# Kernel tuning notes

Measured on AMD Instinct MI355X. Metric: run time of the kernel, lower is better.

The kernel has to match this reference:

```python
import jax, jax.numpy as jnp
import numpy as np

COV_EMB = 32
N_HEAD = 2
FACTOR_TCL = 2   # TemporalConvolutionalLayer factor (default 2)
FACTOR_MLP = 1   # MLP factor passed from MultiAttention init
EPS = 1e-5


def _conv1d_causal(x, w, b):
    # x: [N, C, T], w: [O, C, 3]; torch pads 2 both sides then slices [..., :-2],
    # equivalent to left-pad 2 only -> output length T.
    y = jax.lax.conv_general_dilated(x, w, window_strides=(1,), padding=[(2, 0)],
                                     dimension_numbers=('NCH', 'OIH', 'NCH'))
    return y + b[None, :, None]


def _tcl(x, w_conv, b_conv, w_proj, b_proj):
    # TemporalConvolutionalLayer: x [..., T, C] -> [..., T, C]
    shp = x.shape
    T, C = shp[-2], shp[-1]
    x2 = x.reshape(-1, T, C).transpose(0, 2, 1)              # [N, C, T]
    h = jax.nn.gelu(_conv1d_causal(x2, w_conv, b_conv), approximate=False)
    h = h.transpose(0, 2, 1)                                  # [N, T, 2C]
    out = h @ w_proj.T + b_proj                               # [N, T, C]
    return out.reshape(*shp[:-1], C)


def _layernorm(x, w):
    mu = jnp.mean(x, axis=-1, keepdims=True)
    var = jnp.var(x, axis=-1, keepdims=True)
    return (x - mu) * jax.lax.rsqrt(var + EPS) * w


def setup_inputs() -> dict:
    key = jax.random.key(0)
    ks = jax.random.split(key, 20)
    C = COV_EMB
    C2 = FACTOR_TCL * C
    s = 0.02
    inp = {
        'causal_decoder': jax.random.normal(ks[0], (8, 4, 1024, C), jnp.float32),
        'past_kv': jax.random.normal(ks[1], (8, 1024, C), jnp.float32),
    }
    def tcl_params(i):
        return (jax.random.normal(ks[i], (C2, C, 3), jnp.float32) * s,
                jnp.zeros((C2,), jnp.float32),
                jax.random.normal(ks[i + 1], (C, C2), jnp.float32) * s,
                jnp.zeros((C,), jnp.float32))
    inp['wq_conv'], inp['bq_conv'], inp['wq_proj'], inp['bq_proj'] = tcl_params(2)
    inp['wk_conv'], inp['bk_conv'], inp['wk_proj'], inp['bk_proj'] = tcl_params(4)
    inp['wv_conv'], inp['bv_conv'], inp['wv_proj'], inp['bv_proj'] = tcl_params(6)
    inp['w_cproj'] = jax.random.normal(ks[8], (C, C), jnp.float32) * s   # bias=False
    inp['ln_w'] = jnp.ones((C,), jnp.float32)                            # bias=False
    inp['w_fc'] = jax.random.normal(ks[9], (FACTOR_MLP * C, C), jnp.float32) * s   # bias=False
    inp['w_mlp_proj'] = jax.random.normal(ks[10], (C, FACTOR_MLP * C), jnp.float32) * s
    return inp


def reference(causal_decoder, past_kv,
              wq_conv, bq_conv, wq_proj, bq_proj,
              wk_conv, bk_conv, wk_proj, bk_proj,
              wv_conv, bv_conv, wv_proj, bv_proj,
              w_cproj, ln_w, w_fc, w_mlp_proj):
    B, F, T, C = causal_decoder.shape
    nh, hd = N_HEAD, C // N_HEAD

    q = _tcl(causal_decoder, wq_conv, bq_conv, wq_proj, bq_proj)   # [B,F,T,C]
    k = _tcl(past_kv, wk_conv, bk_conv, wk_proj, bk_proj)          # [B,S,C]
    v = _tcl(past_kv, wv_conv, bv_conv, wv_proj, bv_proj)          # [B,S,C]

    S = k.shape[1]
    q = q.reshape(B, F, T, nh, hd).transpose(0, 1, 3, 2, 4)        # [B,F,h,T,d]
    k = k.reshape(B, S, nh, hd).transpose(0, 2, 1, 3)              # [B,h,S,d]
    v = v.reshape(B, S, nh, hd).transpose(0, 2, 1, 3)              # [B,h,S,d]

    scale = 1.0 / jnp.sqrt(jnp.asarray(hd, q.dtype))
    scores = jnp.einsum('bfhtd,bhsd->bfhts', q, k) * scale          # [B,F,h,T,S]
    attn = jax.nn.softmax(scores, axis=-1)
    y = jnp.einsum('bfhts,bhsd->bfhtd', attn, v)                    # [B,F,h,T,d]
    y = y.transpose(0, 1, 3, 2, 4).reshape(B, F, T, C)

    out = causal_decoder + y @ w_cproj.T                            # resid_dropout = id (p=0)
    h = _layernorm(out, ln_w)
    mlp = jax.nn.gelu(h @ w_fc.T, approximate=False) @ w_mlp_proj.T
    out = out + mlp
    return out
```

## Files before the change

### kernel.cpp

```cpp
#include <hip/hip_runtime.h>

#define T_LEN 1024

typedef __attribute__((ext_vector_type(8))) short short8;
typedef __attribute__((ext_vector_type(4))) short short4v;
typedef __attribute__((ext_vector_type(4))) float float4v;

__device__ __forceinline__ float gelu_exact(float x) {
    return 0.5f * x * (1.0f + erff(x * 0.70710678118654752440f));
}
__device__ __forceinline__ unsigned short f2bf(float f) {
    unsigned u = __float_as_uint(f);
    u += 0x7fffu + ((u >> 16) & 1u);
    return (unsigned short)(u >> 16);
}

__global__ __launch_bounds__(256) void tcl_mfma(
    const float* __restrict__ cd, const float* __restrict__ pkv,
    const float* __restrict__ wqc, const float* __restrict__ bqc,
    const float* __restrict__ wqp, const float* __restrict__ bqp,
    const float* __restrict__ wkc, const float* __restrict__ bkc,
    const float* __restrict__ wkp, const float* __restrict__ bkp,
    const float* __restrict__ wvc, const float* __restrict__ bvc,
    const float* __restrict__ wvp, const float* __restrict__ bvp,
    unsigned short* __restrict__ qbf, unsigned short* __restrict__ kbf,
    unsigned short* __restrict__ vtbf)
{
    __shared__ __align__(16) unsigned short Abuf[64 * 96];
    __shared__ __align__(16) unsigned short WbT[64 * 96];
    __shared__ __align__(16) unsigned short Hb[64 * 72];
    __shared__ __align__(16) unsigned short WpB[32 * 72];

    const int tid = threadIdx.x;
    const int gb = blockIdx.x;

    const float *src, *wc, *bc, *wp, *bp;
    unsigned short* outb;
    int n, mode;
    if (gb < 512)      { n = gb >> 4;          src = cd;  wc = wqc; bc = bqc; wp = wqp; bp = bqp; outb = qbf;  mode = 0; }
    else if (gb < 640) { n = (gb - 512) >> 4;  src = pkv; wc = wkc; bc = bkc; wp = wkp; bp = bkp; outb = kbf;  mode = 0; }
    else               { n = (gb - 640) >> 4;  src = pkv; wc = wvc; bc = bvc; wp = wvp; bp = bvp; outb = vtbf; mode = 1; }
    const int t0 = (gb & 15) * 64;

#pragma unroll
    for (int it = 0; it < 6; ++it) {
        int s = (tid + it * 256) >> 3;
        int sub = tid & 7;
        int t = s / 3, tap = s - t * 3;
        int tau = t0 + t - 2 + tap;
        float4 xv = make_float4(0.f, 0.f, 0.f, 0.f);
        if (tau >= 0) xv = *(const float4*)&src[((size_t)n * T_LEN + tau) * 32 + sub * 4];
        short4v pk = { (short)f2bf(xv.x), (short)f2bf(xv.y),
                       (short)f2bf(xv.z), (short)f2bf(xv.w) };
        *(short4v*)&Abuf[t * 96 + tap * 32 + sub * 4] = pk;
    }
#pragma unroll
    for (int it = 0; it < 6; ++it) {
        int i4 = tid + it * 256;
        int idx = i4 * 4;
        int o = idx / 96, r = idx - o * 96;
        float4 w4 = *(const float4*)&wc[idx];
        float we[4] = { w4.x, w4.y, w4.z, w4.w };
#pragma unroll
        for (int e = 0; e < 4; ++e) {
            int re = r + e, c = re / 3, tap = re - c * 3;
            WbT[o * 96 + tap * 32 + c] = f2bf(we[e]);
        }
    }
#pragma unroll
    for (int it = 0; it < 2; ++it) {
        int i4 = tid + it * 256;
        int idx = i4 * 4;
        int c = idx >> 6, o = idx & 63;
        float4 w4 = *(const float4*)&wp[idx];
        short4v pk = { (short)f2bf(w4.x), (short)f2bf(w4.y),
                       (short)f2bf(w4.z), (short)f2bf(w4.w) };
        *(short4v*)&WpB[c * 72 + o] = pk;
    }

    const int w = tid >> 6;
    const int ln = tid & 63;
    const int sn = ln & 15;
    const int quad = ln >> 4;

    const float bcv = bc[w * 16 + sn];
    const float bp0 = bp[sn], bp1 = bp[16 + sn];

    __syncthreads();

    short8 b0 = *(const short8*)&WbT[(w * 16 + sn) * 96 + 0  + quad * 8];
    short8 b1 = *(const short8*)&WbT[(w * 16 + sn) * 96 + 32 + quad * 8];
    short8 b2 = *(const short8*)&WbT[(w * 16 + sn) * 96 + 64 + quad * 8];
    float4v zero = { 0.f, 0.f, 0.f, 0.f };
    float4v acc[4] = { zero, zero, zero, zero };
#pragma unroll
    for (int tm = 0; tm < 4; ++tm) {
        const unsigned short* ar = &Abuf[(tm * 16 + sn) * 96 + quad * 8];
        short8 a0 = *(const short8*)(ar + 0);
        short8 a1 = *(const short8*)(ar + 32);
        short8 a2 = *(const short8*)(ar + 64);
        acc[tm] = __builtin_amdgcn_mfma_f32_16x16x32_bf16(a0, b0, acc[tm], 0, 0, 0);
        acc[tm] = __builtin_amdgcn_mfma_f32_16x16x32_bf16(a1, b1, acc[tm], 0, 0, 0);
        acc[tm] = __builtin_amdgcn_mfma_f32_16x16x32_bf16(a2, b2, acc[tm], 0, 0, 0);
    }
#pragma unroll
    for (int tm = 0; tm < 4; ++tm) {
        float ge[4];
        ge[0] = gelu_exact(acc[tm].x + bcv);
        ge[1] = gelu_exact(acc[tm].y + bcv);
        ge[2] = gelu_exact(acc[tm].z + bcv);
        ge[3] = gelu_exact(acc[tm].w + bcv);
#pragma unroll
        for (int i = 0; i < 4; ++i)
            Hb[(tm * 16 + quad * 4 + i) * 72 + w * 16 + sn] = f2bf(ge[i]);
    }

    __syncthreads();

    const unsigned short* hr = &Hb[(w * 16 + sn) * 72 + quad * 8];
    short8 pa0 = *(const short8*)(hr + 0);
    short8 pa1 = *(const short8*)(hr + 32);
    short8 pb00 = *(const short8*)&WpB[sn * 72 + quad * 8];
    short8 pb01 = *(const short8*)&WpB[sn * 72 + 32 + quad * 8];
    short8 pb10 = *(const short8*)&WpB[(16 + sn) * 72 + quad * 8];
    short8 pb11 = *(const short8*)&WpB[(16 + sn) * 72 + 32 + quad * 8];
    float4v acc0 = zero, acc1 = zero;
    acc0 = __builtin_amdgcn_mfma_f32_16x16x32_bf16(pa0, pb00, acc0, 0, 0, 0);
    acc0 = __builtin_amdgcn_mfma_f32_16x16x32_bf16(pa1, pb01, acc0, 0, 0, 0);
    acc1 = __builtin_amdgcn_mfma_f32_16x16x32_bf16(pa0, pb10, acc1, 0, 0, 0);
    acc1 = __builtin_amdgcn_mfma_f32_16x16x32_bf16(pa1, pb11, acc1, 0, 0, 0);

    float v0[4] = { acc0.x + bp0, acc0.y + bp0, acc0.z + bp0, acc0.w + bp0 };
    float v1[4] = { acc1.x + bp1, acc1.y + bp1, acc1.z + bp1, acc1.w + bp1 };
#pragma unroll
    for (int i = 0; i < 4; ++i) {
        int t = w * 16 + quad * 4 + i;
        if (mode == 0) {
            size_t rowb = ((size_t)n * T_LEN + t0 + t) * 32;
            outb[rowb + sn]      = f2bf(v0[i]);
            outb[rowb + 16 + sn] = f2bf(v1[i]);
        } else {
            outb[((size_t)(n * 2 + 0) * 16 + sn) * T_LEN + t0 + t] = f2bf(v0[i]);
            outb[((size_t)(n * 2 + 1) * 16 + sn) * T_LEN + t0 + t] = f2bf(v1[i]);
        }
    }
}

__global__ __launch_bounds__(256) void attn_kernel(
    const unsigned short* __restrict__ qbf,
    const unsigned short* __restrict__ kbf,
    const unsigned short* __restrict__ vtbf,
    float* __restrict__ yws)
{
    __shared__ unsigned short plds[4 * 16 * 36];

    const int tid = threadIdx.x;
    const int w = tid >> 6;
    const int ln = tid & 63;
    const int sn = ln & 15;
    const int quad = ln >> 4;
    const int g = blockIdx.x;
    const int tt = g & 15;
    const int bfh = g >> 4;
    const int h = bfh & 1;
    const int bf = bfh >> 1;
    const int b = bf >> 2;
    const int trow = tt * 64 + w * 16 + sn;

    short8 aq = {0, 0, 0, 0, 0, 0, 0, 0};
    if (quad < 2)
        aq = *(const short8*)(qbf + ((size_t)bf * T_LEN + trow) * 32 + h * 16 + quad * 8);

    const unsigned short* kb = kbf + (size_t)b * T_LEN * 32 + h * 16 + quad * 8;
    const unsigned short* vb = vtbf + ((size_t)(b * 2 + h) * 16 + sn) * T_LEN + quad * 8;
    unsigned short* pw = plds + w * 576;

    float4v yacc = {0.f, 0.f, 0.f, 0.f};
    float l0 = 0.f, l1 = 0.f, l2 = 0.f, l3 = 0.f;
    const float SC = 0.36067376022224085f;

#pragma unroll 1
    for (int s0 = 0; s0 < 1024; s0 += 32) {
        short8 bk0 = {0, 0, 0, 0, 0, 0, 0, 0};
        short8 bk1 = {0, 0, 0, 0, 0, 0, 0, 0};
        if (quad < 2) {
            bk0 = *(const short8*)(kb + (size_t)(s0 + sn) * 32);
            bk1 = *(const short8*)(kb + (size_t)(s0 + 16 + sn) * 32);
        }
        float4v z = {0.f, 0.f, 0.f, 0.f};
        float4v c0 = __builtin_amdgcn_mfma_f32_16x16x32_bf16(aq, bk0, z, 0, 0, 0);
        float4v c1 = __builtin_amdgcn_mfma_f32_16x16x32_bf16(aq, bk1, z, 0, 0, 0);

        float p00 = exp2f(c0.x * SC), p01 = exp2f(c0.y * SC);
        float p02 = exp2f(c0.z * SC), p03 = exp2f(c0.w * SC);
        float p10 = exp2f(c1.x * SC), p11 = exp2f(c1.y * SC);
        float p12 = exp2f(c1.z * SC), p13 = exp2f(c1.w * SC);
        l0 += p00 + p10; l1 += p01 + p11;
        l2 += p02 + p12; l3 += p03 + p13;

        const int tb = quad * 4;
        pw[(tb + 0) * 36 + sn]      = f2bf(p00);
        pw[(tb + 1) * 36 + sn]      = f2bf(p01);
        pw[(tb + 2) * 36 + sn]      = f2bf(p02);
        pw[(tb + 3) * 36 + sn]      = f2bf(p03);
        pw[(tb + 0) * 36 + 16 + sn] = f2bf(p10);
        pw[(tb + 1) * 36 + 16 + sn] = f2bf(p11);
        pw[(tb + 2) * 36 + 16 + sn] = f2bf(p12);
        pw[(tb + 3) * 36 + 16 + sn] = f2bf(p13);

        const unsigned short* pr = pw + sn * 36 + quad * 8;
        short4v plo = *(const short4v*)pr;
        short4v phi = *(const short4v*)(pr + 4);
        short8 ap = {plo.x, plo.y, plo.z, plo.w, phi.x, phi.y, phi.z, phi.w};

        short8 bv = *(const short8*)(vb + s0);
        yacc = __builtin_amdgcn_mfma_f32_16x16x32_bf16(ap, bv, yacc, 0, 0, 0);
    }

#pragma unroll
    for (int off = 1; off < 16; off <<= 1) {
        l0 += __shfl_xor(l0, off); l1 += __shfl_xor(l1, off);
        l2 += __shfl_xor(l2, off); l3 += __shfl_xor(l3, off);
    }
    const float i0 = 1.f / l0, i1 = 1.f / l1, i2 = 1.f / l2, i3 = 1.f / l3;

    float* yp = yws + ((size_t)bf * T_LEN + tt * 64 + w * 16 + quad * 4) * 32 + h * 16 + sn;
    yp[0 * 32] = yacc.x * i0;
    yp[1 * 32] = yacc.y * i1;
    yp[2 * 32] = yacc.z * i2;
    yp[3 * 32] = yacc.w * i3;
}

__global__ __launch_bounds__(256) void epi_kernel(
    const float* __restrict__ cd, const float* __restrict__ yws,
    const float* __restrict__ wcp, const float* __restrict__ lnw,
    const float* __restrict__ wfc, const float* __restrict__ wmp,
    float* __restrict__ out)
{
    __shared__ float sy[64][32];
    __shared__ float shn[8][36], sg[8][36];
    __shared__ float sln[32];

    const int tid = threadIdx.x;
    const int rl = tid >> 5, c = tid & 31;

    float wa[32], wb[32], wm[32];
#pragma unroll
    for (int j4 = 0; j4 < 8; ++j4) {
        float4 a = *(const float4*)(wcp + c * 32 + j4 * 4);
        wa[j4 * 4 + 0] = a.x; wa[j4 * 4 + 1] = a.y; wa[j4 * 4 + 2] = a.z; wa[j4 * 4 + 3] = a.w;
        float4 f = *(const float4*)(wfc + c * 32 + j4 * 4);
        wb[j4 * 4 + 0] = f.x; wb[j4 * 4 + 1] = f.y; wb[j4 * 4 + 2] = f.z; wb[j4 * 4 + 3] = f.w;
        float4 m = *(const float4*)(wmp + c * 32 + j4 * 4);
        wm[j4 * 4 + 0] = m.x; wm[j4 * 4 + 1] = m.y; wm[j4 * 4 + 2] = m.z; wm[j4 * 4 + 3] = m.w;
    }
    if (tid < 32) sln[tid] = lnw[tid];

    const size_t base = (size_t)blockIdx.x * 64;
    {
        const float4* ysrc = (const float4*)(yws + base * 32);
        float4* ydst = (float4*)&sy[0][0];
        for (int i = tid; i < 512; i += 256) ydst[i] = ysrc[i];
    }
    __syncthreads();
    const float lnwc = sln[c];

#pragma unroll 1
    for (int p = 0; p < 8; ++p) {
        int r = p * 8 + rl;
        size_t row = base + r;
        float x1 = cd[row * 32 + c];
#pragma unroll
        for (int j4 = 0; j4 < 8; ++j4) {
            float4 yv = *(const float4*)&sy[r][j4 * 4];
            x1 += wa[j4 * 4 + 0] * yv.x + wa[j4 * 4 + 1] * yv.y +
                  wa[j4 * 4 + 2] * yv.z + wa[j4 * 4 + 3] * yv.w;
        }
        float s1 = x1, s2 = x1 * x1;
#pragma unroll
        for (int off = 16; off; off >>= 1) {
            s1 += __shfl_xor(s1, off);
            s2 += __shfl_xor(s2, off);
        }
        float mu = s1 * (1.0f / 32.0f);
        float var = s2 * (1.0f / 32.0f) - mu * mu;
        float hn = (x1 - mu) * rsqrtf(var + 1e-5f) * lnwc;
        shn[rl][c] = hn;
        float ga = 0.f;
#pragma unroll
        for (int j4 = 0; j4 < 8; ++j4) {
            float4 hv = *(const float4*)&shn[rl][j4 * 4];
            ga += wb[j4 * 4 + 0] * hv.x + wb[j4 * 4 + 1] * hv.y +
                  wb[j4 * 4 + 2] * hv.z + wb[j4 * 4 + 3] * hv.w;
        }
        float gv = gelu_exact(ga);
        sg[rl][c] = gv;
        float oa = x1;
#pragma unroll
        for (int j4 = 0; j4 < 8; ++j4) {
            float4 gvv = *(const float4*)&sg[rl][j4 * 4];
            oa += wm[j4 * 4 + 0] * gvv.x + wm[j4 * 4 + 1] * gvv.y +
                  wm[j4 * 4 + 2] * gvv.z + wm[j4 * 4 + 3] * gvv.w;
        }
        out[row * 32 + c] = oa;
    }
}

extern "C" void kernel_launch(void* const* d_in, const int* in_sizes, int n_in,
                              void* d_out, int out_size, void* d_ws, size_t ws_size,
                              hipStream_t stream) {
    const float* cd  = (const float*)d_in[0];
    const float* pkv = (const float*)d_in[1];
    const float* wqc = (const float*)d_in[2];
    const float* bqc = (const float*)d_in[3];
    const float* wqp = (const float*)d_in[4];
    const float* bqp = (const float*)d_in[5];
    const float* wkc = (const float*)d_in[6];
    const float* bkc = (const float*)d_in[7];
    const float* wkp = (const float*)d_in[8];
    const float* bkp = (const float*)d_in[9];
    const float* wvc = (const float*)d_in[10];
    const float* bvc = (const float*)d_in[11];
    const float* wvp = (const float*)d_in[12];
    const float* bvp = (const float*)d_in[13];
    const float* wcp = (const float*)d_in[14];
    const float* lnw = (const float*)d_in[15];
    const float* wfc = (const float*)d_in[16];
    const float* wmp = (const float*)d_in[17];

    unsigned short* qbf  = (unsigned short*)d_ws;
    unsigned short* kbf  = qbf + (size_t)32 * 1024 * 32;
    unsigned short* vtbf = kbf + (size_t)8 * 1024 * 32;
    float* yws = (float*)(vtbf + (size_t)8 * 1024 * 32);

    tcl_mfma<<<768, 256, 0, stream>>>(cd, pkv,
                                      wqc, bqc, wqp, bqp,
                                      wkc, bkc, wkp, bkp,
                                      wvc, bvc, wvp, bvp,
                                      qbf, kbf, vtbf);
    attn_kernel<<<1024, 256, 0, stream>>>(qbf, kbf, vtbf, yws);
    epi_kernel<<<512, 256, 0, stream>>>(cd, yws, wcp, lnw, wfc, wmp, (float*)d_out);
}
```

Before: 145.6 us.

## Split attention key range in two and merge partial sums in epilogue

The attention kernel now splits the 1024-long key dimension into two halves, so twice as many blocks (2048) each run half the loop. Each half writes unnormalized partial outputs and partial softmax denominators to workspace, and the epilogue kernel adds the two halves and normalizes. The aim is more parallelism and a shorter serial loop per block on the attention critical path. The cost is extra workspace traffic for the doubled y buffer plus the denominators. The merge by plain addition is exact only because no running-max subtraction is used.

```diff
diff --git a/kernel.cpp b/kernel.cpp
--- a/kernel.cpp
+++ b/kernel.cpp
@@ -150,7 +150,8 @@
     const unsigned short* __restrict__ qbf,
     const unsigned short* __restrict__ kbf,
     const unsigned short* __restrict__ vtbf,
-    float* __restrict__ yws)
+    float* __restrict__ ynws,
+    float* __restrict__ lws)
 {
     __shared__ unsigned short plds[4 * 16 * 36];
 
@@ -160,8 +161,9 @@
     const int sn = ln & 15;
     const int quad = ln >> 4;
     const int g = blockIdx.x;
-    const int tt = g & 15;
-    const int bfh = g >> 4;
+    const int half = g & 1;
+    const int tt = (g >> 1) & 15;
+    const int bfh = g >> 5;
     const int h = bfh & 1;
     const int bf = bfh >> 1;
     const int b = bf >> 2;
@@ -178,9 +180,10 @@
     float4v yacc = {0.f, 0.f, 0.f, 0.f};
     float l0 = 0.f, l1 = 0.f, l2 = 0.f, l3 = 0.f;
     const float SC = 0.36067376022224085f;
+    const int sbeg = half * 512;
 
 #pragma unroll 1
-    for (int s0 = 0; s0 < 1024; s0 += 32) {
+    for (int s0 = sbeg; s0 < sbeg + 512; s0 += 32) {
         short8 bk0 = {0, 0, 0, 0, 0, 0, 0, 0};
         short8 bk1 = {0, 0, 0, 0, 0, 0, 0, 0};
         if (quad < 2) {
@@ -222,17 +225,21 @@
         l0 += __shfl_xor(l0, off); l1 += __shfl_xor(l1, off);
         l2 += __shfl_xor(l2, off); l3 += __shfl_xor(l3, off);
     }
-    const float i0 = 1.f / l0, i1 = 1.f / l1, i2 = 1.f / l2, i3 = 1.f / l3;
-
-    float* yp = yws + ((size_t)bf * T_LEN + tt * 64 + w * 16 + quad * 4) * 32 + h * 16 + sn;
-    yp[0 * 32] = yacc.x * i0;
-    yp[1 * 32] = yacc.y * i1;
-    yp[2 * 32] = yacc.z * i2;
-    yp[3 * 32] = yacc.w * i3;
+
+    float* yp = ynws + (((size_t)half * 32 + bf) * T_LEN + tt * 64 + w * 16 + quad * 4) * 32 + h * 16 + sn;
+    yp[0 * 32] = yacc.x;
+    yp[1 * 32] = yacc.y;
+    yp[2 * 32] = yacc.z;
+    yp[3 * 32] = yacc.w;
+    if (sn == 0) {
+        float* lp = lws + (((size_t)half * 32 + bf) * 2 + h) * T_LEN + tt * 64 + w * 16 + quad * 4;
+        lp[0] = l0; lp[1] = l1; lp[2] = l2; lp[3] = l3;
+    }
 }
 
 __global__ __launch_bounds__(256) void epi_kernel(
-    const float* __restrict__ cd, const float* __restrict__ yws,
+    const float* __restrict__ cd, const float* __restrict__ ynws,
+    const float* __restrict__ lws,
     const float* __restrict__ wcp, const float* __restrict__ lnw,
     const float* __restrict__ wfc, const float* __restrict__ wmp,
     float* __restrict__ out)
@@ -256,11 +263,26 @@
     }
     if (tid < 32) sln[tid] = lnw[tid];
 
+    const int bf = blockIdx.x >> 4;
+    const int t0 = (blockIdx.x & 15) * 64;
     const size_t base = (size_t)blockIdx.x * 64;
     {
-        const float4* ysrc = (const float4*)(yws + base * 32);
+        const float4* yn0 = (const float4*)ynws;
+        const float4* yn1 = (const float4*)(ynws + (size_t)32 * T_LEN * 32);
         float4* ydst = (float4*)&sy[0][0];
-        for (int i = tid; i < 512; i += 256) ydst[i] = ysrc[i];
+        for (int i = tid; i < 512; i += 256) {
+            int r = i >> 3, c4 = i & 7, hh = c4 >> 2;
+            int t = t0 + r;
+            float l = lws[((size_t)bf * 2 + hh) * T_LEN + t] +
+                      lws[(((size_t)32 + bf) * 2 + hh) * T_LEN + t];
+            float inv = 1.0f / l;
+            float4 a = yn0[base * 8 + i];
+            float4 b = yn1[base * 8 + i];
+            float4 v;
+            v.x = (a.x + b.x) * inv; v.y = (a.y + b.y) * inv;
+            v.z = (a.z + b.z) * inv; v.w = (a.w + b.w) * inv;
+            ydst[i] = v;
+        }
     }
     __syncthreads();
     const float lnwc = sln[c];
@@ -331,13 +353,15 @@
     unsigned short* qbf  = (unsigned short*)d_ws;
     unsigned short* kbf  = qbf + (size_t)32 * 1024 * 32;
     unsigned short* vtbf = kbf + (size_t)8 * 1024 * 32;
-    float* yws = (float*)(vtbf + (size_t)8 * 1024 * 32);
+    float* ynws = (float*)(vtbf + (size_t)8 * 1024 * 32);
+    float* lws  = ynws + (size_t)2 * 32 * 1024 * 32;
 
     tcl_mfma<<<768, 256, 0, stream>>>(cd, pkv,
                                       wqc, bqc, wqp, bqp,
                                       wkc, bkc, wkp, bkp,
                                       wvc, bvc, wvp, bvp,
                                       qbf, kbf, vtbf);
-    attn_kernel<<<1024, 256, 0, stream>>>(qbf, kbf, vtbf, yws);
-    epi_kernel<<<512, 256, 0, stream>>>(cd, yws, wcp, lnw, wfc, wmp, (float*)d_out);
-}
+    attn_kernel<<<2048, 256, 0, stream>>>(qbf, kbf, vtbf, ynws, lws);
+    epi_kernel<<<512, 256, 0, stream>>>(cd, ynws, lws, wcp, lnw, wfc, wmp,
+                                        (float*)d_out);
+}
```

Measured after the change: 146.8 us. Within noise of the previous version (+0.9%).

## Halve TCL time tile to double blocks; unroll attention loop over 64 keys

Applied to the files above, without the earlier changes.

The TCL kernel now handles 32 time steps per block instead of 64, so it launches twice as many blocks. The projection GEMM work is split across the four waves by time-half and channel-half. The attention loop handles 64 keys per iteration, issuing four QK MFMAs and two PV MFMAs with separate LDS staging buffers so more loads and exps are in flight at once. The costs are that each TCL block reloads the conv weights for half the work, and the attention loop uses more registers and LDS.

```diff
diff --git a/kernel.cpp b/kernel.cpp
--- a/kernel.cpp
+++ b/kernel.cpp
@@ -26,9 +26,9 @@
     unsigned short* __restrict__ qbf, unsigned short* __restrict__ kbf,
     unsigned short* __restrict__ vtbf)
 {
-    __shared__ __align__(16) unsigned short Abuf[64 * 96];
+    __shared__ __align__(16) unsigned short Abuf[32 * 96];
     __shared__ __align__(16) unsigned short WbT[64 * 96];
-    __shared__ __align__(16) unsigned short Hb[64 * 72];
+    __shared__ __align__(16) unsigned short Hb[32 * 72];
     __shared__ __align__(16) unsigned short WpB[32 * 72];
 
     const int tid = threadIdx.x;
@@ -37,13 +37,13 @@
     const float *src, *wc, *bc, *wp, *bp;
     unsigned short* outb;
     int n, mode;
-    if (gb < 512)      { n = gb >> 4;          src = cd;  wc = wqc; bc = bqc; wp = wqp; bp = bqp; outb = qbf;  mode = 0; }
-    else if (gb < 640) { n = (gb - 512) >> 4;  src = pkv; wc = wkc; bc = bkc; wp = wkp; bp = bkp; outb = kbf;  mode = 0; }
-    else               { n = (gb - 640) >> 4;  src = pkv; wc = wvc; bc = bvc; wp = wvp; bp = bvp; outb = vtbf; mode = 1; }
-    const int t0 = (gb & 15) * 64;
-
-#pragma unroll
-    for (int it = 0; it < 6; ++it) {
+    if (gb < 1024)      { n = gb >> 5;           src = cd;  wc = wqc; bc = bqc; wp = wqp; bp = bqp; outb = qbf;  mode = 0; }
+    else if (gb < 1280) { n = (gb - 1024) >> 5;  src = pkv; wc = wkc; bc = bkc; wp = wkp; bp = bkp; outb = kbf;  mode = 0; }
+    else                { n = (gb - 1280) >> 5;  src = pkv; wc = wvc; bc = bvc; wp = wvp; bp = bvp; outb = vtbf; mode = 1; }
+    const int t0 = (gb & 31) * 32;
+
+#pragma unroll
+    for (int it = 0; it < 3; ++it) {
         int s = (tid + it * 256) >> 3;
         int sub = tid & 7;
         int t = s / 3, tap = s - t * 3;
@@ -84,7 +84,8 @@
     const int quad = ln >> 4;
 
     const float bcv = bc[w * 16 + sn];
-    const float bp0 = bp[sn], bp1 = bp[16 + sn];
+    const int tmw = w & 1, cnw = w >> 1;
+    const float bpv = bp[cnw * 16 + sn];
 
     __syncthreads();
 
@@ -92,9 +93,9 @@
     short8 b1 = *(const short8*)&WbT[(w * 16 + sn) * 96 + 32 + quad * 8];
     short8 b2 = *(const short8*)&WbT[(w * 16 + sn) * 96 + 64 + quad * 8];
     float4v zero = { 0.f, 0.f, 0.f, 0.f };
-    float4v acc[4] = { zero, zero, zero, zero };
-#pragma unroll
-    for (int tm = 0; tm < 4; ++tm) {
+    float4v acc[2] = { zero, zero };
+#pragma unroll
+    for (int tm = 0; tm < 2; ++tm) {
         const unsigned short* ar = &Abuf[(tm * 16 + sn) * 96 + quad * 8];
         short8 a0 = *(const short8*)(ar + 0);
         short8 a1 = *(const short8*)(ar + 32);
@@ -104,7 +105,7 @@
         acc[tm] = __builtin_amdgcn_mfma_f32_16x16x32_bf16(a2, b2, acc[tm], 0, 0, 0);
     }
 #pragma unroll
-    for (int tm = 0; tm < 4; ++tm) {
+    for (int tm = 0; tm < 2; ++tm) {
         float ge[4];
         ge[0] = gelu_exact(acc[tm].x + bcv);
         ge[1] = gelu_exact(acc[tm].y + bcv);
@@ -117,31 +118,24 @@
 
     __syncthreads();
 
-    const unsigned short* hr = &Hb[(w * 16 + sn) * 72 + quad * 8];
+    const unsigned short* hr = &Hb[(tmw * 16 + sn) * 72 + quad * 8];
     short8 pa0 = *(const short8*)(hr + 0);
     short8 pa1 = *(const short8*)(hr + 32);
-    short8 pb00 = *(const short8*)&WpB[sn * 72 + quad * 8];
-    short8 pb01 = *(const short8*)&WpB[sn * 72 + 32 + quad * 8];
-    short8 pb10 = *(const short8*)&WpB[(16 + sn) * 72 + quad * 8];
-    short8 pb11 = *(const short8*)&WpB[(16 + sn) * 72 + 32 + quad * 8];
-    float4v acc0 = zero, acc1 = zero;
-    acc0 = __builtin_amdgcn_mfma_f32_16x16x32_bf16(pa0, pb00, acc0, 0, 0, 0);
-    acc0 = __builtin_amdgcn_mfma_f32_16x16x32_bf16(pa1, pb01, acc0, 0, 0, 0);
-    acc1 = __builtin_amdgcn_mfma_f32_16x16x32_bf16(pa0, pb10, acc1, 0, 0, 0);
-    acc1 = __builtin_amdgcn_mfma_f32_16x16x32_bf16(pa1, pb11, acc1, 0, 0, 0);
-
-    float v0[4] = { acc0.x + bp0, acc0.y + bp0, acc0.z + bp0, acc0.w + bp0 };
-    float v1[4] = { acc1.x + bp1, acc1.y + bp1, acc1.z + bp1, acc1.w + bp1 };
+    short8 pb0 = *(const short8*)&WpB[(cnw * 16 + sn) * 72 + quad * 8];
+    short8 pb1 = *(const short8*)&WpB[(cnw * 16 + sn) * 72 + 32 + quad * 8];
+    float4v pacc = zero;
+    pacc = __builtin_amdgcn_mfma_f32_16x16x32_bf16(pa0, pb0, pacc, 0, 0, 0);
+    pacc = __builtin_amdgcn_mfma_f32_16x16x32_bf16(pa1, pb1, pacc, 0, 0, 0);
+
+    float v[4] = { pacc.x + bpv, pacc.y + bpv, pacc.z + bpv, pacc.w + bpv };
 #pragma unroll
     for (int i = 0; i < 4; ++i) {
-        int t = w * 16 + quad * 4 + i;
+        int t = tmw * 16 + quad * 4 + i;
+        int c = cnw * 16 + sn;
         if (mode == 0) {
-            size_t rowb = ((size_t)n * T_LEN + t0 + t) * 32;
-            outb[rowb + sn]      = f2bf(v0[i]);
-            outb[rowb + 16 + sn] = f2bf(v1[i]);
+            outb[((size_t)n * T_LEN + t0 + t) * 32 + c] = f2bf(v[i]);
         } else {
-            outb[((size_t)(n * 2 + 0) * 16 + sn) * T_LEN + t0 + t] = f2bf(v0[i]);
-            outb[((size_t)(n * 2 + 1) * 16 + sn) * T_LEN + t0 + t] = f2bf(v1[i]);
+            outb[((size_t)(n * 2 + cnw) * 16 + sn) * T_LEN + t0 + t] = f2bf(v[i]);
         }
     }
 }
@@ -152,7 +146,7 @@
     const unsigned short* __restrict__ vtbf,
     float* __restrict__ yws)
 {
-    __shared__ unsigned short plds[4 * 16 * 36];
+    __shared__ unsigned short plds[4 * 2 * 16 * 36];
 
     const int tid = threadIdx.x;
     const int w = tid >> 6;
@@ -173,48 +167,74 @@
 
     const unsigned short* kb = kbf + (size_t)b * T_LEN * 32 + h * 16 + quad * 8;
     const unsigned short* vb = vtbf + ((size_t)(b * 2 + h) * 16 + sn) * T_LEN + quad * 8;
-    unsigned short* pw = plds + w * 576;
+    unsigned short* pwA = plds + w * 1152;
+    unsigned short* pwB = pwA + 576;
 
     float4v yacc = {0.f, 0.f, 0.f, 0.f};
     float l0 = 0.f, l1 = 0.f, l2 = 0.f, l3 = 0.f;
     const float SC = 0.36067376022224085f;
 
 #pragma unroll 1
-    for (int s0 = 0; s0 < 1024; s0 += 32) {
-        short8 bk0 = {0, 0, 0, 0, 0, 0, 0, 0};
-        short8 bk1 = {0, 0, 0, 0, 0, 0, 0, 0};
+    for (int s0 = 0; s0 < 1024; s0 += 64) {
+        short8 ka0 = {0,0,0,0,0,0,0,0}, ka1 = ka0, kb0 = ka0, kb1 = ka0;
         if (quad < 2) {
-            bk0 = *(const short8*)(kb + (size_t)(s0 + sn) * 32);
-            bk1 = *(const short8*)(kb + (size_t)(s0 + 16 + sn) * 32);
-        }
+            ka0 = *(const short8*)(kb + (size_t)(s0 + sn) * 32);
+            ka1 = *(const short8*)(kb + (size_t)(s0 + 16 + sn) * 32);
+            kb0 = *(const short8*)(kb + (size_t)(s0 + 32 + sn) * 32);
+            kb1 = *(const short8*)(kb + (size_t)(s0 + 48 + sn) * 32);
+        }
+        short8 bvA = *(const short8*)(vb + s0);
+        short8 bvB = *(const short8*)(vb + s0 + 32);
+
         float4v z = {0.f, 0.f, 0.f, 0.f};
-        float4v c0 = __builtin_amdgcn_mfma_f32_16x16x32_bf16(aq, bk0, z, 0, 0, 0);
-        float4v c1 = __builtin_amdgcn_mfma_f32_16x16x32_bf16(aq, bk1, z, 0, 0, 0);
-
-        float p00 = exp2f(c0.x * SC), p01 = exp2f(c0.y * SC);
-        float p02 = exp2f(c0.z * SC), p03 = exp2f(c0.w * SC);
-        float p10 = exp2f(c1.x * SC), p11 = exp2f(c1.y * SC);
-        float p12 = exp2f(c1.z * SC), p13 = exp2f(c1.w * SC);
-        l0 += p00 + p10; l1 += p01 + p11;
-        l2 += p02 + p12; l3 += p03 + p13;
+        float4v cA0 = __builtin_amdgcn_mfma_f32_16x16x32_bf16(aq, ka0, z, 0, 0, 0);
+        float4v cA1 = __builtin_amdgcn_mfma_f32_16x16x32_bf16(aq, ka1, z, 0, 0, 0);
+        float4v cB0 = __builtin_amdgcn_mfma_f32_16x16x32_bf16(aq, kb0, z, 0, 0, 0);
+        float4v cB1 = __builtin_amdgcn_mfma_f32_16x16x32_bf16(aq, kb1, z, 0, 0, 0);
+
+        float pA00 = exp2f(cA0.x * SC), pA01 = exp2f(cA0.y * SC);
+        float pA02 = exp2f(cA0.z * SC), pA03 = exp2f(cA0.w * SC);
+        float pA10 = exp2f(cA1.x * SC), pA11 = exp2f(cA1.y * SC);
+        float pA12 = exp2f(cA1.z * SC), pA13 = exp2f(cA1.w * SC);
+        float pB00 = exp2f(cB0.x * SC), pB01 = exp2f(cB0.y * SC);
+        float pB02 = exp2f(cB0.z * SC), pB03 = exp2f(cB0.w * SC);
+        float pB10 = exp2f(cB1.x * SC), pB11 = exp2f(cB1.y * SC);
+        float pB12 = exp2f(cB1.z * SC), pB13 = exp2f(cB1.w * SC);
+
+        l0 += (pA00 + pA10) + (pB00 + pB10);
+        l1 += (pA01 + pA11) + (pB01 + pB11);
+        l2 += (pA02 + pA12) + (pB02 + pB12);
+        l3 += (pA03 + pA13) + (pB03 + pB13);
 
         const int tb = quad * 4;
-        pw[(tb + 0) * 36 + sn]      = f2bf(p00);
-        pw[(tb + 1) * 36 + sn]      = f2bf(p01);
-        pw[(tb + 2) * 36 + sn]      = f2bf(p02);
-        pw[(tb + 3) * 36 + sn]      = f2bf(p03);
-        pw[(tb + 0) * 36 + 16 + sn] = f2bf(p10);
-        pw[(tb + 1) * 36 + 16 + sn] = f2bf(p11);
-        pw[(tb + 2) * 36 + 16 + sn] = f2bf(p12);
-        pw[(tb + 3) * 36 + 16 + sn] = f2bf(p13);
-
-        const unsigned short* pr = pw + sn * 36 + quad * 8;
-        short4v plo = *(const short4v*)pr;
-        short4v phi = *(const short4v*)(pr + 4);
-        short8 ap = {plo.x, plo.y, plo.z, plo.w, phi.x, phi.y, phi.z, phi.w};
-
-        short8 bv = *(const short8*)(vb + s0);
-        yacc = __builtin_amdgcn_mfma_f32_16x16x32_bf16(ap, bv, yacc, 0, 0, 0);
+        pwA[(tb + 0) * 36 + sn]      = f2bf(pA00);
+        pwA[(tb + 1) * 36 + sn]      = f2bf(pA01);
+        pwA[(tb + 2) * 36 + sn]      = f2bf(pA02);
+        pwA[(tb + 3) * 36 + sn]      = f2bf(pA03);
+        pwA[(tb + 0) * 36 + 16 + sn] = f2bf(pA10);
+        pwA[(tb + 1) * 36 + 16 + sn] = f2bf(pA11);
+        pwA[(tb + 2) * 36 + 16 + sn] = f2bf(pA12);
+        pwA[(tb + 3) * 36 + 16 + sn] = f2bf(pA13);
+        pwB[(tb + 0) * 36 + sn]      = f2bf(pB00);
+        pwB[(tb + 1) * 36 + sn]      = f2bf(pB01);
+        pwB[(tb + 2) * 36 + sn]      = f2bf(pB02);
+        pwB[(tb + 3) * 36 + sn]      = f2bf(pB03);
+        pwB[(tb + 0) * 36 + 16 + sn] = f2bf(pB10);
+        pwB[(tb + 1) * 36 + 16 + sn] = f2bf(pB11);
+        pwB[(tb + 2) * 36 + 16 + sn] = f2bf(pB12);
+        pwB[(tb + 3) * 36 + 16 + sn] = f2bf(pB13);
+
+        const unsigned short* prA = pwA + sn * 36 + quad * 8;
+        const unsigned short* prB = pwB + sn * 36 + quad * 8;
+        short4v aloA = *(const short4v*)prA;
+        short4v ahiA = *(const short4v*)(prA + 4);
+        short4v aloB = *(const short4v*)prB;
+        short4v ahiB = *(const short4v*)(prB + 4);
+        short8 apA = {aloA.x, aloA.y, aloA.z, aloA.w, ahiA.x, ahiA.y, ahiA.z, ahiA.w};
+        short8 apB = {aloB.x, aloB.y, aloB.z, aloB.w, ahiB.x, ahiB.y, ahiB.z, ahiB.w};
+
+        yacc = __builtin_amdgcn_mfma_f32_16x16x32_bf16(apA, bvA, yacc, 0, 0, 0);
+        yacc = __builtin_amdgcn_mfma_f32_16x16x32_bf16(apB, bvB, yacc, 0, 0, 0);
     }
 
 #pragma unroll
@@ -333,11 +353,11 @@
     unsigned short* vtbf = kbf + (size_t)8 * 1024 * 32;
     float* yws = (float*)(vtbf + (size_t)8 * 1024 * 32);
 
-    tcl_mfma<<<768, 256, 0, stream>>>(cd, pkv,
-                                      wqc, bqc, wqp, bqp,
-                                      wkc, bkc, wkp, bkp,
-                                      wvc, bvc, wvp, bvp,
-                                      qbf, kbf, vtbf);
+    tcl_mfma<<<1536, 256, 0, stream>>>(cd, pkv,
+                                       wqc, bqc, wqp, bqp,
+                                       wkc, bkc, wkp, bkp,
+                                       wvc, bvc, wvp, bvp,
+                                       qbf, kbf, vtbf);
     attn_kernel<<<1024, 256, 0, stream>>>(qbf, kbf, vtbf, yws);
     epi_kernel<<<512, 256, 0, stream>>>(cd, yws, wcp, lnw, wfc, wmp, (float*)d_out);
 }
```

Result: no change. 143.9 us (-1.2%).
